# Kernel optimization log

Hardware: AMD Instinct MI355X
Metric: run time of the kernel (lower is better)

The kernel has to match this reference:

```python
import jax, jax.numpy as jnp
import numpy as np
from jax import lax

BEAM = 4
MAXLEN = 12
V, E, H = 32000, 256, 512
S, B = 512, 8


def lstm_cell(x, h, c, Wih, Whh, bih, bhh):
    # torch gate order: input, forget, cell, output
    g = x @ Wih.T + h @ Whh.T + bih + bhh
    i, f, gg, o = jnp.split(g, 4, axis=-1)
    c2 = jax.nn.sigmoid(f) * c + jax.nn.sigmoid(i) * jnp.tanh(gg)
    return jax.nn.sigmoid(o) * jnp.tanh(c2), c2


def lstm_layer(xs, Wih, Whh, bih, bhh):
    Bn, Hn = xs.shape[1], Whh.shape[1]
    h0 = jnp.zeros((Bn, Hn), xs.dtype)

    def step(carry, x):
        h, c = carry
        h, c = lstm_cell(x, h, c, Wih, Whh, bih, bhh)
        return (h, c), h

    (hT, cT), hs = lax.scan(step, (h0, h0), xs)
    return hs, hT, cT


def setup_inputs():
    key = jax.random.key(0)
    ks = jax.random.split(key, 32)

    def p(i, shape, s=0.08):
        return jax.random.normal(ks[i], shape, jnp.float32) * s

    return {
        'text': jax.random.randint(ks[0], (S, B), 0, V),
        'emb_enc': p(1, (V, E)),
        'emb_dec': p(2, (V, E)),
        'enc_Wih0': p(3, (4 * H, E)), 'enc_Whh0': p(4, (4 * H, H)),
        'enc_bih0': p(5, (4 * H,)), 'enc_bhh0': p(6, (4 * H,)),
        'enc_Wih1': p(7, (4 * H, H)), 'enc_Whh1': p(8, (4 * H, H)),
        'enc_bih1': p(9, (4 * H,)), 'enc_bhh1': p(10, (4 * H,)),
        'dec_Wih': p(11, (4 * H, E)), 'dec_Whh': p(12, (4 * H, H)),
        'dec_bih': p(13, (4 * H,)), 'dec_bhh': p(14, (4 * H,)),
        'Wq': p(15, (H, H)), 'bq': p(16, (H,)),
        'Wk': p(17, (H, H)), 'bk': p(18, (H,)),
        'Wv': p(19, (H, H)), 'bv': p(20, (H,)),
        'Wo': p(21, (H, H)), 'bo': p(22, (H,)),
        'Wout': p(23, (V, H)), 'bout': p(24, (V,)),
    }


def reference(text, emb_enc, emb_dec, enc_Wih0, enc_Whh0, enc_bih0, enc_bhh0,
              enc_Wih1, enc_Whh1, enc_bih1, enc_bhh1,
              dec_Wih, dec_Whh, dec_bih, dec_bhh,
              Wq, bq, Wk, bk, Wv, bv, Wo, bo, Wout, bout):
    # ---- encoder: 2-layer LSTM over source ----
    emb = emb_enc[text]                                   # [S, B, E]
    hs0, h0, c0 = lstm_layer(emb, enc_Wih0, enc_Whh0, enc_bih0, enc_bhh0)
    hs1, h1, c1 = lstm_layer(hs0, enc_Wih1, enc_Whh1, enc_bih1, enc_bhh1)
    enc_hidden = jnp.stack([h0, h1])                      # [L, B, H] final hidden per layer
    k_enc = enc_hidden @ Wk.T + bk                        # precompute encoder K/V projections
    v_enc = enc_hidden @ Wv.T + bv
    scale = 1.0 / jnp.sqrt(jnp.float32(H))

    # ---- beam state: all beams start from last encoder layer state ----
    dec_h = jnp.tile(h1[None], (BEAM, 1, 1))              # [BEAM, B, H]
    dec_c = jnp.tile(c1[None], (BEAM, 1, 1))
    T = MAXLEN + 1
    result = jnp.full((BEAM, T, B), 1, dtype=jnp.int32)   # SOS token = 1
    logits_hist = jnp.zeros((BEAM, T, B, V), jnp.float32).at[:, 0, :, 1].set(1.0)

    def step(carry, t):
        dh, dc, res, lh = carry
        tok = lax.dynamic_slice(res, (0, t, 0), (BEAM, 1, B))[:, 0, :]      # last token [BEAM, B]
        x = emb_dec[tok]                                                    # [BEAM, B, E]
        nh, nc = lstm_cell(x, dh, dc, dec_Wih, dec_Whh, dec_bih, dec_bhh)   # batched over beams
        # single-head attention: query = dec hidden, keys/values = [enc layers ; dec hidden]
        q = nh @ Wq.T + bq
        kd = nh @ Wk.T + bk
        vd = nh @ Wv.T + bv
        keys = jnp.concatenate([jnp.broadcast_to(k_enc[None], (BEAM,) + k_enc.shape), kd[:, None]], axis=1)  # [BEAM, L+1, B, H]
        vals = jnp.concatenate([jnp.broadcast_to(v_enc[None], (BEAM,) + v_enc.shape), vd[:, None]], axis=1)
        scores = jnp.einsum('nbh,nlbh->nbl', q, keys) * scale
        w = jax.nn.softmax(scores, axis=-1)
        ctx = jnp.einsum('nbl,nlbh->nbh', w, vals)
        dec_out = (ctx @ Wo.T + bo) @ Wout.T + bout                          # [BEAM, B, V]
        # per-beam top-k over vocab, then top-k over the BEAM*BEAM candidates
        pv, pt = lax.top_k(dec_out, BEAM)                                    # [BEAM, B, K]
        cand_v = jnp.transpose(pv, (1, 0, 2)).reshape(B, BEAM * BEAM)        # beam-major blocks
        cand_t = jnp.transpose(pt, (1, 0, 2)).reshape(B, BEAM * BEAM)
        _, ti = lax.top_k(cand_v, BEAM)                                      # [B, K]
        old_beam = (ti // BEAM).T                                            # [BEAM, B]
        new_tok = jnp.take_along_axis(cand_t, ti, axis=1).T                  # [BEAM, B]
        # vectorized beam reorder (gather) of state + history
        nh = jnp.take_along_axis(nh, old_beam[:, :, None], axis=0)
        nc = jnp.take_along_axis(nc, old_beam[:, :, None], axis=0)
        res = jnp.take_along_axis(res, old_beam[:, None, :], axis=0)
        lh = jnp.take_along_axis(lh, old_beam[:, None, :, None], axis=0)
        step_log = jnp.take_along_axis(dec_out, old_beam[:, :, None], axis=0)
        res = lax.dynamic_update_slice(res, new_tok[:, None, :].astype(jnp.int32), (0, t + 1, 0))
        lh = lax.dynamic_update_slice(lh, step_log[:, None], (0, t + 1, 0, 0))
        return (nh, nc, res, lh), None

    (dec_h, dec_c, result, logits_hist), _ = lax.scan(
        step, (dec_h, dec_c, result, logits_hist), jnp.arange(MAXLEN))
    output_res = result[0].T                               # [B, T]
    output_logits = jnp.transpose(logits_hist[0], (1, 2, 0))  # [B, V, T]
    return output_res, output_logits
```

## Files before the change

### kernel.cpp

```cpp
#include <hip/hip_runtime.h>
#include <hip/hip_bf16.h>
#include <float.h>


using ull = unsigned long long;

#define SCOPE_AGENT __HIP_MEMORY_SCOPE_AGENT

__device__ __forceinline__ float cLoad(const float* p) {
  return __hip_atomic_load(p, __ATOMIC_RELAXED, SCOPE_AGENT);
}
__device__ __forceinline__ void cStore(float* p, float v) {
  __hip_atomic_store(p, v, __ATOMIC_RELAXED, SCOPE_AGENT);
}
__device__ __forceinline__ int cLoadI(const int* p) {
  return __hip_atomic_load(p, __ATOMIC_RELAXED, SCOPE_AGENT);
}
__device__ __forceinline__ void cStoreI(int* p, int v) {
  __hip_atomic_store(p, v, __ATOMIC_RELAXED, SCOPE_AGENT);
}
__device__ __forceinline__ ull cLoad64(const ull* p) {
  return __hip_atomic_load(p, __ATOMIC_RELAXED, SCOPE_AGENT);
}
__device__ __forceinline__ void cStore64(ull* p, ull v) {
  __hip_atomic_store(p, v, __ATOMIC_RELAXED, SCOPE_AGENT);
}

__device__ __forceinline__ float2 u2f2(ull u) {
  union { ull u; float2 f; } c; c.u = u; return c.f;
}

__device__ __forceinline__ ull pollLoad(const ull* p) {
  ull v = cLoad64(p);
  while ((unsigned)v == 0xFFFFFFFFu || (unsigned)(v >> 32) == 0xFFFFFFFFu)
    v = cLoad64(p);
  return v;
}

__device__ __forceinline__ void fbar1(int* fl, int phase) {
  __syncthreads();
  if (threadIdx.x < 32)
    cStoreI(fl + (blockIdx.x * 32 + threadIdx.x) * 32, phase);
  {
    const int* f = fl + (threadIdx.x * 32 + (blockIdx.x >> 3)) * 32;
    while (cLoadI(f) < phase) {}
  }
  __syncthreads();
}

__device__ __forceinline__ float sig_(float x) { return 1.0f / (1.0f + expf(-x)); }

__device__ __forceinline__ void ins4(float* v, int* id, float nv, int ni) {
  if (nv > v[3] || (nv == v[3] && ni < id[3])) {
    v[3] = nv; id[3] = ni;
#pragma unroll
    for (int p = 3; p > 0; --p) {
      bool sw = (v[p] > v[p - 1]) || (v[p] == v[p - 1] && id[p] < id[p - 1]);
      if (sw) {
        float t0 = v[p]; v[p] = v[p - 1]; v[p - 1] = t0;
        int t1 = id[p]; id[p] = id[p - 1]; id[p - 1] = t1;
      }
    }
  }
}

struct EncP {
  const int* text; const float* emb;
  const float* Wih0; const float* Whh0; const float* bih0; const float* bhh0;
  const float* Wih1; const float* Whh1; const float* bih1; const float* bhh1;
  float* h0hist; float* h1hist;
  float* h0f; float* h1f; float* c1f;
};

template <int KX>
__device__ void enc_run(const EncP& P, float* xcat, int w, int tid) {
  constexpr int KTOT = KX + 512;
  constexpr int ST = KTOT + 4;
  constexpr int KSL = KTOT / 8;
  constexpr int Q = KSL / 4;
  constexpr int L = (KX == 512) ? 1 : 0;
  __shared__ float part[16 * 8 * 8];
  __shared__ float gl[128];

  const int c0 = (w & 127) * 4;
  const int kh = tid >> 5, col = (tid >> 3) & 3, b = tid & 7;
  const int kbase = kh * KSL;

  const float* Wih = L ? P.Wih1 : P.Wih0;
  const float* Whh = L ? P.Whh1 : P.Whh0;
  const float4* wih4[4]; const float4* whh4[4];
#pragma unroll
  for (int g = 0; g < 4; ++g) {
    const int row = g * 512 + c0 + col;
    wih4[g] = (const float4*)(Wih + (size_t)row * KX);
    whh4[g] = (const float4*)(Whh + (size_t)row * 512);
  }
  float bsum = 0.f;
  if (tid < 128) {
    const int r = tid >> 3;
    const int row = (r & 3) * 512 + c0 + (r >> 2);
    bsum = (L ? P.bih1[row] + P.bhh1[row] : P.bih0[row] + P.bhh0[row]);
  }
  float creg = 0.f;
  float* myHist = L ? P.h1hist : P.h0hist;

  int qx = (KX - kbase) / 4;
  qx = qx < 0 ? 0 : (qx > Q ? Q : qx);

  for (int e = tid; e < 4096; e += 256)
    xcat[(e >> 9) * ST + KX + (e & 511)] = 0.f;
  __syncthreads();

  for (int t = 0; t < 512; ++t) {
    if constexpr (KX == 256) {
      for (int e = tid; e < 1024; e += 256) {
        const int b2 = e >> 7, k2 = e & 127;
        const int tokv = P.text[t * 8 + b2];
        *(float2*)(xcat + b2 * ST + 2 * k2) =
            *(const float2*)(P.emb + (size_t)tokv * 256 + 2 * k2);
      }
    } else {
      const ull* x0 = (const ull*)(P.h0hist + (size_t)(t + 1) * 4096);
      for (int e = tid; e < 2048; e += 256) {
        const int b2 = e >> 8, k2 = e & 255;
        *(ull*)(xcat + b2 * ST + 2 * k2) = pollLoad(x0 + b2 * 256 + k2);
      }
    }
    if (t >= 1) {
      const ull* hq = (const ull*)(myHist + (size_t)t * 4096);
      for (int e = tid; e < 2048; e += 256) {
        const int b2 = e >> 8, k2 = e & 255;
        *(ull*)(xcat + b2 * ST + KX + 2 * k2) = pollLoad(hq + b2 * 256 + k2);
      }
    }
    __syncthreads();

    float a0 = 0.f, a1 = 0.f, a2 = 0.f, a3 = 0.f;
    {
      const float4* xq = (const float4*)(xcat + b * ST + kbase);
      const int iw = kbase >> 2, ih = (kbase - KX) >> 2;
#pragma unroll 4
      for (int q = 0; q < qx; ++q) {
        float4 x = xq[q];
        float4 w0 = wih4[0][iw + q], w1 = wih4[1][iw + q];
        float4 w2 = wih4[2][iw + q], w3 = wih4[3][iw + q];
        a0 = fmaf(w0.x, x.x, a0); a0 = fmaf(w0.y, x.y, a0);
        a0 = fmaf(w0.z, x.z, a0); a0 = fmaf(w0.w, x.w, a0);
        a1 = fmaf(w1.x, x.x, a1); a1 = fmaf(w1.y, x.y, a1);
        a1 = fmaf(w1.z, x.z, a1); a1 = fmaf(w1.w, x.w, a1);
        a2 = fmaf(w2.x, x.x, a2); a2 = fmaf(w2.y, x.y, a2);
        a2 = fmaf(w2.z, x.z, a2); a2 = fmaf(w2.w, x.w, a2);
        a3 = fmaf(w3.x, x.x, a3); a3 = fmaf(w3.y, x.y, a3);
        a3 = fmaf(w3.z, x.z, a3); a3 = fmaf(w3.w, x.w, a3);
      }
#pragma unroll 4
      for (int q = qx; q < Q; ++q) {
        float4 x = xq[q];
        float4 w0 = whh4[0][ih + q], w1 = whh4[1][ih + q];
        float4 w2 = whh4[2][ih + q], w3 = whh4[3][ih + q];
        a0 = fmaf(w0.x, x.x, a0); a0 = fmaf(w0.y, x.y, a0);
        a0 = fmaf(w0.z, x.z, a0); a0 = fmaf(w0.w, x.w, a0);
        a1 = fmaf(w1.x, x.x, a1); a1 = fmaf(w1.y, x.y, a1);
        a1 = fmaf(w1.z, x.z, a1); a1 = fmaf(w1.w, x.w, a1);
        a2 = fmaf(w2.x, x.x, a2); a2 = fmaf(w2.y, x.y, a2);
        a2 = fmaf(w2.z, x.z, a2); a2 = fmaf(w2.w, x.w, a2);
        a3 = fmaf(w3.x, x.x, a3); a3 = fmaf(w3.y, x.y, a3);
        a3 = fmaf(w3.z, x.z, a3); a3 = fmaf(w3.w, x.w, a3);
      }
    }
    part[((col * 4 + 0) * 8 + b) * 8 + kh] = a0;
    part[((col * 4 + 1) * 8 + b) * 8 + kh] = a1;
    part[((col * 4 + 2) * 8 + b) * 8 + kh] = a2;
    part[((col * 4 + 3) * 8 + b) * 8 + kh] = a3;
    __syncthreads();
    if (tid < 128) {
      const int r = tid >> 3, b2 = tid & 7;
      const float4* pp = (const float4*)(part + (r * 8 + b2) * 8);
      float4 p0 = pp[0], p1 = pp[1];
      gl[r * 8 + b2] =
          bsum + (((p0.x + p0.y) + (p0.z + p0.w)) + ((p1.x + p1.y) + (p1.z + p1.w)));
    }
    __syncthreads();
    if (tid < 32) {
      const int cc = tid >> 3, b2 = tid & 7;
      float gi = gl[(cc * 4 + 0) * 8 + b2], gf_ = gl[(cc * 4 + 1) * 8 + b2];
      float gg = gl[(cc * 4 + 2) * 8 + b2], go = gl[(cc * 4 + 3) * 8 + b2];
      float c2 = sig_(gf_) * creg + sig_(gi) * tanhf(gg);
      float hv = sig_(go) * tanhf(c2);
      creg = c2;
      cStore(myHist + (size_t)(t + 1) * 4096 + b2 * 512 + c0 + cc, hv);
      if (t == 511) {
        (L ? P.h1f : P.h0f)[b2 * 512 + c0 + cc] = hv;
        if (L) P.c1f[b2 * 512 + c0 + cc] = c2;
      }
    }
    __syncthreads();
  }
}

__global__ __launch_bounds__(256, 1) void enc_kernel(EncP P) {
  __shared__ float xcat0[8 * 772];
  __shared__ float xcat1[8 * 1028];
  if (blockIdx.x >> 7) enc_run<512>(P, xcat1, blockIdx.x, threadIdx.x);
  else enc_run<256>(P, xcat0, blockIdx.x, threadIdx.x);
}

__global__ __launch_bounds__(256) void prep_kernel(
    const float* Wk, const float* bk, const float* Wv, const float* bv,
    const float* h0f, const float* h1f, const float* c1f,
    float* kenc, float* venc, float* nhb, float* ncb) {
  const int w = blockIdx.x, tid = threadIdx.x;
  if (w < 64) {
    const int o = w * 256 + tid;
    const int kv = o >> 13, l = (o >> 12) & 1, b = (o >> 9) & 7, c = o & 511;
    const float4* h4 = (const float4*)((l ? h1f : h0f) + b * 512);
    const float4* w4 = (const float4*)((kv ? Wv : Wk) + (size_t)c * 512);
    float s0 = 0.f, s1 = 0.f, s2 = 0.f, s3 = 0.f;
#pragma unroll 8
    for (int k = 0; k < 128; ++k) {
      float4 a = w4[k], x = h4[k];
      s0 = fmaf(a.x, x.x, s0); s1 = fmaf(a.y, x.y, s1);
      s2 = fmaf(a.z, x.z, s2); s3 = fmaf(a.w, x.w, s3);
    }
    (kv ? venc : kenc)[l * 4096 + b * 512 + c] =
        (kv ? bv : bk)[c] + ((s0 + s1) + (s2 + s3));
  } else {
    const int o = (w - 64) * 256 + tid;
    nhb[16384 + o] = h1f[o & 4095];
    ncb[16384 + o] = c1f[o & 4095];
  }
}

__global__ __launch_bounds__(256) void prep2_kernel(
    const float* Wq, const float* Wk, const float* Wv, const float* Wo,
    const float* bq, const float* bk, const float* bv,
    const float* kenc, const float* venc,
    float* At, float* W2, float* u, float* pvec, float* veWo, float* bvo,
    float* sl0, float* sbb) {
  const int w = blockIdx.x, tid = threadIdx.x;
#pragma unroll 1
  for (int sub = 0; sub < 2; ++sub) {
    const int d = 2 * w + sub;
    for (int cc = 0; cc < 2; ++cc) {
      const int c = tid + cc * 256;
      float s0 = 0.f, s1 = 0.f, s2 = 0.f, s3 = 0.f;
      for (int i = 0; i < 512; i += 4) {
        s0 = fmaf(Wk[(i + 0) * 512 + d], Wq[(i + 0) * 512 + c], s0);
        s1 = fmaf(Wk[(i + 1) * 512 + d], Wq[(i + 1) * 512 + c], s1);
        s2 = fmaf(Wk[(i + 2) * 512 + d], Wq[(i + 2) * 512 + c], s2);
        s3 = fmaf(Wk[(i + 3) * 512 + d], Wq[(i + 3) * 512 + c], s3);
      }
      At[(size_t)d * 512 + c] = (s0 + s1) + (s2 + s3);
    }
    for (int cc = 0; cc < 2; ++cc) {
      const int dc = tid + cc * 256;
      float s0 = 0.f, s1 = 0.f, s2 = 0.f, s3 = 0.f;
      const float* wor = Wo + (size_t)d * 512;
      for (int c2 = 0; c2 < 512; c2 += 4) {
        s0 = fmaf(wor[c2 + 0], Wv[(size_t)(c2 + 0) * 512 + dc], s0);
        s1 = fmaf(wor[c2 + 1], Wv[(size_t)(c2 + 1) * 512 + dc], s1);
        s2 = fmaf(wor[c2 + 2], Wv[(size_t)(c2 + 2) * 512 + dc], s2);
        s3 = fmaf(wor[c2 + 3], Wv[(size_t)(c2 + 3) * 512 + dc], s3);
      }
      W2[(size_t)d * 512 + dc] = (s0 + s1) + (s2 + s3);
    }
  }
  if (w == 0) {
    for (int cc = 0; cc < 2; ++cc) {
      const int c = tid + cc * 256;
      float a = 0.f;
      for (int i = 0; i < 512; ++i)
        a += Wq[i * 512 + c] * bk[i] + Wk[i * 512 + c] * bq[i];
      u[c] = a;
    }
  } else if (w <= 32) {
    const int idx = (w - 1) * 256 + tid;
    const int l = idx >> 12, b = (idx >> 9) & 7, c = idx & 511;
    const float* ke = kenc + l * 4096 + b * 512;
    float a = 0.f;
    for (int i = 0; i < 512; ++i) a = fmaf(Wq[i * 512 + c], ke[i], a);
    pvec[idx] = a;
  } else if (w <= 64) {
    const int idx = (w - 33) * 256 + tid;
    const int l = idx >> 12, b = (idx >> 9) & 7, j = idx & 511;
    const float* ve = venc + l * 4096 + b * 512;
    const float* wo = Wo + (size_t)j * 512;
    float a = 0.f;
    for (int c = 0; c < 512; ++c) a = fmaf(wo[c], ve[c], a);
    veWo[idx] = a;
  } else if (w == 65) {
    for (int cc = 0; cc < 2; ++cc) {
      const int j = tid + cc * 256;
      const float* wo = Wo + (size_t)j * 512;
      float a = 0.f;
      for (int c = 0; c < 512; ++c) a = fmaf(wo[c], bv[c], a);
      bvo[j] = a;
    }
  } else if (w == 66) {
    if (tid < 16) {
      const int l = tid >> 3, b = tid & 7;
      const float* ke = kenc + l * 4096 + b * 512;
      float a = 0.f;
      for (int i = 0; i < 512; ++i) a = fmaf(bq[i], ke[i], a);
      sl0[tid] = a;
    } else if (tid == 16) {
      float a = 0.f;
      for (int i = 0; i < 512; ++i) a = fmaf(bq[i], bk[i], a);
      sbb[0] = a;
    }
  }
}

__global__ __launch_bounds__(256) void prep3_kernel(
    const float* Wout, const float* bout, const float* bo, const float* veWo,
    float* E0g, float* E1g, float* bcg) {
  __shared__ float sv[16 * 516 + 512];
  __shared__ float stg[8 * 516];
  const int w = blockIdx.x, tid = threadIdx.x;
  for (int e = tid; e < 8704; e += 256) {
    if (e < 8192) sv[(e >> 9) * 516 + (e & 511)] = veWo[e];
    else sv[16 * 516 + (e - 8192)] = bo[e - 8192];
  }
  const int cbase = w * 125;
  for (int tile = 0; tile < 16; ++tile) {
    const int r0 = tile * 8;
    __syncthreads();
    for (int e = tid; e < 1024; e += 256) {
      const int rr = e >> 7, k4 = e & 127;
      int row = r0 + rr; if (row > 124) row = 124;
      *(float4*)&stg[rr * 516 + k4 * 4] =
          *(const float4*)&Wout[(size_t)(cbase + row) * 512 + k4 * 4];
    }
    __syncthreads();
    if (tid < 136) {
      const int rr = tid / 17, sel = tid - rr * 17;
      const int row = r0 + rr;
      if (row < 125) {
        const float4* a4 = (const float4*)&stg[rr * 516];
        const float4* x4 =
            (const float4*)&sv[sel < 16 ? sel * 516 : 16 * 516];
        float s0 = 0.f, s1 = 0.f, s2 = 0.f, s3 = 0.f;
#pragma unroll 8
        for (int k = 0; k < 128; ++k) {
          float4 a = a4[k], x = x4[k];
          s0 = fmaf(a.x, x.x, s0); s1 = fmaf(a.y, x.y, s1);
          s2 = fmaf(a.z, x.z, s2); s3 = fmaf(a.w, x.w, s3);
        }
        const float s = (s0 + s1) + (s2 + s3);
        const int c = cbase + row;
        if (sel < 16) (sel < 8 ? E0g : E1g)[(size_t)(sel & 7) * 32000 + c] = s;
        else bcg[c] = s + bout[c];
      }
    }
  }
}

struct DecP {
  const float* emb;
  const float* Wih; const float* Whh; const float* bih; const float* bhh;
  const float* Wout;
  const float* At; const float* W2; const float* u; const float* bvo;
  const float* pvec; const float* sl0; const float* sbb;
  const float* E0g; const float* E1g; const float* bcg;
  float* nhb; float* ncb;
  float* vbuf;
  float* part_s;
  ull* pvp;
  int* obh;
  int* res0;
  __hip_bfloat16* hist;
  int* fl;
};

__global__ __launch_bounds__(256, 1) void dec_kernel(DecP P) {
  __shared__ float SM[29600];
  __shared__ float gl[2][4][32];
  __shared__ float slS[32][3];
  __shared__ float wslS[96];
  __shared__ float svv[32][8][4];
  __shared__ int sii[32][8][4];
  __shared__ float rvS[32][4];
  __shared__ int rtS[32][4];
  __shared__ int resS[4][13][8];
  __shared__ int oblS[32];
  __shared__ int tokS[32];
  __shared__ float pscS[32][8];
  __shared__ float nhsS[32][8];

  const int w = blockIdx.x, tid = threadIdx.x;
  float* hs = SM;
  float* tileS = SM;
  float* vqS = SM + 16896;
  float* tvE = SM + 21120;
  int* tiE = (int*)(SM + 25344);
  int ph = 0;

  if (tid < 104) {
    for (int n = 0; n < 4; ++n) resS[n][tid >> 3][tid & 7] = 1;
  }

  auto do_select = [&](int tt) {
    {
      const int r = tid >> 3, ch = tid & 7;
      float m4[4] = {-FLT_MAX, -FLT_MAX, -FLT_MAX, -FLT_MAX};
      int mi[4] = {0x7fffffff, 0x7fffffff, 0x7fffffff, 0x7fffffff};
      for (int g = 0; g < 4; ++g) {
        ull pk[32];
#pragma unroll
        for (int z = 0; z < 32; ++z) {
          const int wg = ch * 32 + g * 8 + (z >> 2);
          pk[z] = cLoad64(P.pvp + wg * 128 + r * 4 + (z & 3));
        }
#pragma unroll
        for (int z = 0; z < 32; ++z)
          ins4(m4, mi, __uint_as_float((unsigned)(pk[z] >> 32)),
               (int)(unsigned)(pk[z] & 0xffffffffu));
      }
#pragma unroll
      for (int k = 0; k < 4; ++k) { svv[r][ch][k] = m4[k]; sii[r][ch][k] = mi[k]; }
    }
    __syncthreads();
    if (tid < 32) {
      float m4[4] = {-FLT_MAX, -FLT_MAX, -FLT_MAX, -FLT_MAX};
      int mi[4] = {0x7fffffff, 0x7fffffff, 0x7fffffff, 0x7fffffff};
      for (int g2 = 0; g2 < 8; ++g2)
#pragma unroll
        for (int k = 0; k < 4; ++k) ins4(m4, mi, svv[tid][g2][k], sii[tid][g2][k]);
#pragma unroll
      for (int k = 0; k < 4; ++k) { rvS[tid][k] = m4[k]; rtS[tid][k] = mi[k]; }
    }
    __syncthreads();
    if (tid < 8) {
      const int b2 = tid;
      unsigned used = 0;
      int obl_[4], tkl_[4];
#pragma unroll
      for (int sel = 0; sel < 4; ++sel) {
        float bestv = -FLT_MAX; int bestj = -1;
        for (int j = 0; j < 16; ++j) {
          if (used & (1u << j)) continue;
          float vv = rvS[(j >> 2) * 8 + b2][j & 3];
          if (vv > bestv) { bestv = vv; bestj = j; }
        }
        used |= 1u << bestj;
        const int obn = bestj >> 2;
        obl_[sel] = obn;
        tkl_[sel] = rtS[obn * 8 + b2][bestj & 3];
        oblS[sel * 8 + b2] = obn;
        tokS[sel * 8 + b2] = tkl_[sel];
        if (w == 0) P.obh[tt * 32 + sel * 8 + b2] = obn;
      }
      if (w == 0) {
        int tmp[4][13];
        for (int n2 = 0; n2 < 4; ++n2)
          for (int s2 = 0; s2 < 13; ++s2) tmp[n2][s2] = resS[obl_[n2]][s2][b2];
        for (int n2 = 0; n2 < 4; ++n2)
          for (int s2 = 0; s2 < 13; ++s2) resS[n2][s2][b2] = tmp[n2][s2];
        for (int n2 = 0; n2 < 4; ++n2) resS[n2][tt + 1][b2] = tkl_[n2];
      }
    }
    __syncthreads();
    if (tt == 11 && w == 0 && tid < 104)
      P.res0[tid] = resS[0][tid >> 3][tid & 7];
  };

  for (int t = 0; t < 12; ++t) {
    const int curOff = (t & 1) * 16384, prevOff = ((t + 1) & 1) * 16384;

    if (t == 0) {
      __syncthreads();
      if (tid < 32) { oblS[tid] = tid >> 3; tokS[tid] = 1; }
      __syncthreads();
    } else {
      do_select(t - 1);
    }
    {
      const int col_l = tid >> 7, gate = (tid >> 5) & 3, nb = tid & 31;
      const int col = 2 * w + col_l;
      const int row = gate * 512 + col;
      for (int e = tid; e < 2048; e += 256) {
        const int nb2 = e >> 6, kf = e & 63;
        float4 v = *((const float4*)(P.emb + (size_t)tokS[nb2] * 256) + kf);
        *((float4*)hs + nb2 * 65 + kf) = v;
      }
      __syncthreads();
      float s0 = 0.f, s1 = 0.f, s2 = 0.f, s3 = 0.f;
      {
        const float4* a4 = (const float4*)(P.Wih + (size_t)row * 256);
        const float4* x4 = (const float4*)hs + nb * 65;
#pragma unroll 8
        for (int k = 0; k < 64; ++k) {
          float4 a = a4[k], x = x4[k];
          s0 = fmaf(a.x, x.x, s0); s1 = fmaf(a.y, x.y, s1);
          s2 = fmaf(a.z, x.z, s2); s3 = fmaf(a.w, x.w, s3);
        }
      }
      float acc = P.bih[row] + P.bhh[row];
      const ull* hsrc = (const ull*)(P.nhb + prevOff);
      const float4* w4row = (const float4*)(P.Whh + (size_t)row * 512);
      for (int ck = 0; ck < 2; ++ck) {
        __syncthreads();
        for (int e = tid; e < 4096; e += 256) {
          const int nb2 = e >> 7, k2 = e & 127;
          const int srow = oblS[nb2] * 8 + (nb2 & 7);
          ull v = cLoad64(hsrc + srow * 256 + ck * 128 + k2);
          *(ull*)(hs + nb2 * 260 + 2 * k2) = v;
        }
        __syncthreads();
        const float4* h4 = (const float4*)hs + nb * 65;
        const float4* w4 = w4row + ck * 64;
#pragma unroll 8
        for (int k = 0; k < 64; ++k) {
          float4 a = w4[k], x = h4[k];
          s0 = fmaf(a.x, x.x, s0); s1 = fmaf(a.y, x.y, s1);
          s2 = fmaf(a.z, x.z, s2); s3 = fmaf(a.w, x.w, s3);
        }
      }
      acc += (s0 + s1) + (s2 + s3);
      gl[col_l][gate][nb] = acc;
      __syncthreads();
      if (tid < 64) {
        const int cc = tid >> 5, nb2 = tid & 31;
        const int col2 = 2 * w + cc;
        float gi = gl[cc][0][nb2], gf_ = gl[cc][1][nb2];
        float gg = gl[cc][2][nb2], go = gl[cc][3][nb2];
        const int srow = oblS[nb2] * 8 + (nb2 & 7);
        float cold = cLoad(P.ncb + prevOff + srow * 512 + col2);
        float c2 = sig_(gf_) * cold + sig_(gi) * tanhf(gg);
        float hv = sig_(go) * tanhf(c2);
        cStore(P.nhb + curOff + nb2 * 512 + col2, hv);
        cStore(P.ncb + curOff + nb2 * 512 + col2, c2);
      }
    }
    fbar1(P.fl, ++ph);

    if (w < 128) {
      const int p = w >> 6, cb = w & 63;
      const int col_l = tid >> 5, nb = tid & 31;
      const int col = cb * 8 + col_l;
      const float* W = (p ? P.W2 : P.At) + (size_t)col * 512;
      float acc = (p ? P.bvo : P.u)[col];
      {
        const float4* w4row = (const float4*)W;
        float s0 = 0.f, s1 = 0.f, s2 = 0.f, s3 = 0.f;
        for (int ck = 0; ck < 2; ++ck) {
          __syncthreads();
          const ull* s8 = (const ull*)(P.nhb + curOff);
          for (int e = tid; e < 4096; e += 256) {
            const int nb2 = e >> 7, k2 = e & 127;
            ull v = cLoad64(s8 + nb2 * 256 + ck * 128 + k2);
            *(ull*)(hs + nb2 * 260 + 2 * k2) = v;
          }
          __syncthreads();
          const float4* h4 = (const float4*)hs + nb * 65;
          const float4* w4 = w4row + ck * 64;
#pragma unroll 8
          for (int k = 0; k < 64; ++k) {
            float4 a = w4[k], x = h4[k];
            s0 = fmaf(a.x, x.x, s0); s1 = fmaf(a.y, x.y, s1);
            s2 = fmaf(a.z, x.z, s2); s3 = fmaf(a.w, x.w, s3);
          }
        }
        acc += (s0 + s1) + (s2 + s3);
      }
      if (p) {
        cStore(P.vbuf + nb * 512 + col, acc);
      } else {
        const float nhv = cLoad(P.nhb + curOff + nb * 512 + col);
        pscS[nb][col_l] = nhv * acc;
        nhsS[nb][col_l] = nhv;
        __syncthreads();
        if (tid < 32) {
          const int nb2 = tid, b = nb2 & 7;
          float s2a = 0.f, l0 = 0.f, l1 = 0.f;
#pragma unroll
          for (int i2 = 0; i2 < 8; ++i2) {
            s2a += pscS[nb2][i2];
            const float nv = nhsS[nb2][i2];
            l0 = fmaf(nv, P.pvec[b * 512 + cb * 8 + i2], l0);
            l1 = fmaf(nv, P.pvec[4096 + b * 512 + cb * 8 + i2], l1);
          }
          cStore(P.part_s + (0 * 32 + nb2) * 64 + cb, l0);
          cStore(P.part_s + (1 * 32 + nb2) * 64 + cb, l1);
          cStore(P.part_s + (2 * 32 + nb2) * 64 + cb, s2a);
        }
      }
    }
    fbar1(P.fl, ++ph);

    {
      const int cbase = w * 125;
      if (tid < 96) {
        const int nb = tid / 3, l = tid - (tid / 3) * 3, b = nb & 7;
        const ull* ps = (const ull*)(P.part_s + (l * 32 + nb) * 64);
        ull pk[32];
#pragma unroll
        for (int z = 0; z < 32; ++z) pk[z] = cLoad64(ps + z);
        float s = 0.f;
#pragma unroll
        for (int z = 0; z < 32; ++z) { float2 f = u2f2(pk[z]); s += f.x + f.y; }
        const float bias = (l < 2) ? P.sl0[l * 8 + b] : P.sbb[0];
        slS[nb][l] = (s + bias) * (1.0f / sqrtf(512.0f));
      }
      __syncthreads();
      if (tid < 32) {
        float a = slS[tid][0], b2 = slS[tid][1], c3 = slS[tid][2];
        float m = fmaxf(a, fmaxf(b2, c3));
        float e0 = expf(a - m), e1 = expf(b2 - m), e2 = expf(c3 - m);
        float inv = 1.0f / (e0 + e1 + e2);
        wslS[tid * 3 + 0] = e0 * inv;
        wslS[tid * 3 + 1] = e1 * inv;
        wslS[tid * 3 + 2] = e2 * inv;
      }
      const int rg = tid >> 3, ng = tid & 7;
      float acc[4][4];
#pragma unroll
      for (int i = 0; i < 4; ++i)
#pragma unroll
        for (int j = 0; j < 4; ++j) acc[i][j] = 0.f;
      for (int q = 0; q < 4; ++q) {
        __syncthreads();
        for (int e = tid; e < 1024; e += 256) {
          const int nb = e >> 5, kf = e & 31;
          ull u0 = cLoad64((const ull*)(P.vbuf + nb * 512 + q * 128 + kf * 4));
          ull u1 = cLoad64((const ull*)(P.vbuf + nb * 512 + q * 128 + kf * 4 + 2));
          float2 a = u2f2(u0), b2 = u2f2(u1);
          float4 v = {a.x, a.y, b2.x, b2.y};
          *(float4*)(vqS + (nb & 3) * 1056 + (nb >> 2) * 132 + kf * 4) = v;
        }
        for (int it = 0; it < 16; ++it) {
          const int idx = it * 256 + tid;
          if (idx < 4000) {
            const int r = idx >> 5, kf = idx & 31;
            float4 v = *(const float4*)(P.Wout + (size_t)(cbase + r) * 512 +
                                        q * 128 + kf * 4);
            *(float4*)(tileS + (r & 3) * 4224 + (r >> 2) * 132 + kf * 4) = v;
          }
        }
        __syncthreads();
        for (int kf = 0; kf < 32; ++kf) {
          float4 xv[4], wv[4];
#pragma unroll
          for (int j = 0; j < 4; ++j)
            xv[j] = *(const float4*)(vqS + j * 1056 + ng * 132 + kf * 4);
#pragma unroll
          for (int i = 0; i < 4; ++i)
            wv[i] = *(const float4*)(tileS + i * 4224 + rg * 132 + kf * 4);
#pragma unroll
          for (int i = 0; i < 4; ++i)
#pragma unroll
            for (int j = 0; j < 4; ++j) {
              float a = acc[i][j];
              a = fmaf(wv[i].x, xv[j].x, a); a = fmaf(wv[i].y, xv[j].y, a);
              a = fmaf(wv[i].z, xv[j].z, a); a = fmaf(wv[i].w, xv[j].w, a);
              acc[i][j] = a;
            }
        }
      }
      __syncthreads();
      float w0w[4], w1w[4], w2w[4];
#pragma unroll
      for (int j = 0; j < 4; ++j) {
        const int nb = ng * 4 + j;
        w0w[j] = wslS[nb * 3 + 0]; w1w[j] = wslS[nb * 3 + 1]; w2w[j] = wslS[nb * 3 + 2];
      }
      float v4[4][4]; int i4[4][4];
#pragma unroll
      for (int j = 0; j < 4; ++j)
#pragma unroll
        for (int k = 0; k < 4; ++k) { v4[j][k] = -FLT_MAX; i4[j][k] = 0x7fffffff; }
#pragma unroll
      for (int i = 0; i < 4; ++i) {
        const int r = rg * 4 + i;
        if (r < 125) {
          const int c = cbase + r;
          const float bcv = P.bcg[c];
#pragma unroll
          for (int j = 0; j < 4; ++j) {
            const int nb = ng * 4 + j, b = nb & 7;
            const float e0 = P.E0g[(size_t)b * 32000 + c];
            const float e1 = P.E1g[(size_t)b * 32000 + c];
            const float L = fmaf(w2w[j], acc[i][j],
                                 fmaf(w0w[j], e0, fmaf(w1w[j], e1, bcv)));
            P.hist[(size_t)t * 1024000 + (size_t)nb * 32000 + c] = __float2bfloat16(L);
            ins4(v4[j], i4[j], L, c);
          }
        }
      }
#pragma unroll
      for (int j = 0; j < 4; ++j)
#pragma unroll
        for (int k = 0; k < 4; ++k) {
          tvE[(ng * 4 + j) * 132 + rg * 4 + k] = v4[j][k];
          tiE[(ng * 4 + j) * 132 + rg * 4 + k] = i4[j][k];
        }
      __syncthreads();
      if (tid < 32) {
        float m4[4] = {-FLT_MAX, -FLT_MAX, -FLT_MAX, -FLT_MAX};
        int mi[4] = {0x7fffffff, 0x7fffffff, 0x7fffffff, 0x7fffffff};
        for (int e = 0; e < 128; ++e)
          ins4(m4, mi, tvE[tid * 132 + e], tiE[tid * 132 + e]);
#pragma unroll
        for (int k = 0; k < 4; ++k) {
          ull pk = ((ull)__float_as_uint(m4[k]) << 32) | (unsigned)mi[k];
          cStore64(P.pvp + w * 128 + tid * 4 + k, pk);
        }
      }
    }
    fbar1(P.fl, ++ph);
  }
  if (w == 0) do_select(11);
}

__global__ __launch_bounds__(256) void out_kernel(const __hip_bfloat16* hist,
                                                  const int* obh, const int* res0,
                                                  float* out) {
  __shared__ float sh[13 * 1000];
  __shared__ int sbArr[12];
  const int w = blockIdx.x, tid = threadIdx.x;
  const int b = w >> 5, v0 = (w & 31) * 1000;
  if (tid == 0) {
    int beta = 0;
    for (int t = 11; t >= 0; --t) {
      const int sb = obh[t * 32 + beta * 8 + b];
      sbArr[t] = sb;
      beta = sb;
    }
  }
  __syncthreads();
  for (int e = tid; e < 12000; e += 256) {
    const int t = e / 1000, vv = e - t * 1000;
    sh[(t + 1) * 1000 + vv] = __bfloat162float(
        hist[(size_t)(t * 32 + sbArr[t] * 8 + b) * 32000 + v0 + vv]);
  }
  for (int e = tid; e < 1000; e += 256) sh[e] = (v0 + e == 1) ? 1.0f : 0.0f;
  __syncthreads();
  float* base = out + 104 + (size_t)(b * 32000 + v0) * 13;
  for (int o = tid; o < 13000; o += 256) {
    const int v = o / 13, t = o - v * 13;
    base[o] = sh[t * 1000 + v];
  }
  if (w == 0 && tid < 104) {
    out[(tid & 7) * 13 + (tid >> 3)] = (float)res0[tid];
  }
}

extern "C" void kernel_launch(void* const* d_in, const int* in_sizes, int n_in,
                              void* d_out, int out_size, void* d_ws, size_t ws_size,
                              hipStream_t stream) {
  const int* text  = (const int*)d_in[0];
  const float* embE = (const float*)d_in[1];
  const float* embD = (const float*)d_in[2];
  const float* Wih0 = (const float*)d_in[3];
  const float* Whh0 = (const float*)d_in[4];
  const float* bih0 = (const float*)d_in[5];
  const float* bhh0 = (const float*)d_in[6];
  const float* Wih1 = (const float*)d_in[7];
  const float* Whh1 = (const float*)d_in[8];
  const float* bih1 = (const float*)d_in[9];
  const float* bhh1 = (const float*)d_in[10];
  const float* dWih = (const float*)d_in[11];
  const float* dWhh = (const float*)d_in[12];
  const float* dbih = (const float*)d_in[13];
  const float* dbhh = (const float*)d_in[14];
  const float* Wq = (const float*)d_in[15];
  const float* bq = (const float*)d_in[16];
  const float* Wk = (const float*)d_in[17];
  const float* bk = (const float*)d_in[18];
  const float* Wv = (const float*)d_in[19];
  const float* bv = (const float*)d_in[20];
  const float* Wo = (const float*)d_in[21];
  const float* bo = (const float*)d_in[22];
  const float* Wout = (const float*)d_in[23];
  const float* bout = (const float*)d_in[24];

  char* ws = (char*)d_ws;
  size_t off = 0;
  auto alloc = [&](size_t bytes) -> char* {
    off = (off + 511) & ~(size_t)511;
    char* p = ws + off;
    off += bytes;
    return p;
  };
  float* h0hist = (float*)alloc((size_t)513 * 4096 * 4);
  float* h1hist = (float*)alloc((size_t)513 * 4096 * 4);
  int* decFl  = (int*)alloc((size_t)262144 * 4);
  float* h0f  = (float*)alloc(4096 * 4);
  float* h1f  = (float*)alloc(4096 * 4);
  float* c1f  = (float*)alloc(4096 * 4);
  float* kenc = (float*)alloc(8192 * 4);
  float* venc = (float*)alloc(8192 * 4);
  float* At   = (float*)alloc((size_t)262144 * 4);
  float* W2   = (float*)alloc((size_t)262144 * 4);
  float* u    = (float*)alloc(512 * 4);
  float* pvec = (float*)alloc(8192 * 4);
  float* veWo = (float*)alloc(8192 * 4);
  float* bvo  = (float*)alloc(512 * 4);
  float* sl0  = (float*)alloc(16 * 4);
  float* sbb  = (float*)alloc(32 * 4);
  float* E0g  = (float*)alloc((size_t)256000 * 4);
  float* E1g  = (float*)alloc((size_t)256000 * 4);
  float* bcg  = (float*)alloc(32000 * 4);
  float* nhb  = (float*)alloc(2 * 16384 * 4);
  float* ncb  = (float*)alloc(2 * 16384 * 4);
  float* vbuf = (float*)alloc(16384 * 4);
  float* part_s = (float*)alloc(6144 * 4);
  ull* pvp    = (ull*)alloc((size_t)32768 * 8);
  int* obh    = (int*)alloc(384 * 4);
  int* res0   = (int*)alloc(104 * 4);
  __hip_bfloat16* hist = (__hip_bfloat16*)alloc((size_t)12288000 * 2);
  if (off > ws_size) return;

  hipMemsetAsync(h0hist, 0xFF, (size_t)513 * 4096 * 4, stream);
  hipMemsetAsync(h1hist, 0xFF, (size_t)513 * 4096 * 4, stream);
  hipMemsetAsync(decFl, 0, (size_t)262144 * 4, stream);

  EncP ep{text, embE, Wih0, Whh0, bih0, bhh0, Wih1, Whh1, bih1, bhh1,
          h0hist, h1hist, h0f, h1f, c1f};
  enc_kernel<<<256, 256, 0, stream>>>(ep);

  prep_kernel<<<128, 256, 0, stream>>>(Wk, bk, Wv, bv, h0f, h1f, c1f, kenc, venc,
                                       nhb, ncb);
  prep2_kernel<<<256, 256, 0, stream>>>(Wq, Wk, Wv, Wo, bq, bk, bv, kenc, venc,
                                        At, W2, u, pvec, veWo, bvo, sl0, sbb);
  prep3_kernel<<<256, 256, 0, stream>>>(Wout, bout, bo, veWo, E0g, E1g, bcg);

  DecP dp{embD, dWih, dWhh, dbih, dbhh, Wout,
          At, W2, u, bvo, pvec, sl0, sbb, E0g, E1g, bcg,
          nhb, ncb, vbuf, part_s, pvp, obh, res0, hist, decFl};
  dec_kernel<<<256, 256, 0, stream>>>(dp);

  out_kernel<<<256, 256, 0, stream>>>(hist, obh, res0, (float*)d_out);
}
```

Measured before the change: 6.623 ms.

## Replace sentinel polling with flag barrier and replicated double-buffered hidden state

The encoder's per-element sentinel polling on a 513-step history buffer is replaced with a flag-based global barrier. Hidden states now go into small double-buffered arrays, replicated 16x for layer 0 and 8x for layer 1, so groups of blocks read separate copies and contention drops. Layer 1 runs one step behind layer 0 in lockstep. The k-split reduction moves from shared-memory partials plus two syncthreads to intra-wavefront shuffles. In exchange, each block does more global stores per step and every step waits on a full barrier.

```diff
diff --git a/kernel.cpp b/kernel.cpp
--- a/kernel.cpp
+++ b/kernel.cpp
@@ -28,13 +28,6 @@
 
 __device__ __forceinline__ float2 u2f2(ull u) {
   union { ull u; float2 f; } c; c.u = u; return c.f;
-}
-
-__device__ __forceinline__ ull pollLoad(const ull* p) {
-  ull v = cLoad64(p);
-  while ((unsigned)v == 0xFFFFFFFFu || (unsigned)(v >> 32) == 0xFFFFFFFFu)
-    v = cLoad64(p);
-  return v;
 }
 
 __device__ __forceinline__ void fbar1(int* fl, int phase) {
@@ -68,7 +61,7 @@
   const int* text; const float* emb;
   const float* Wih0; const float* Whh0; const float* bih0; const float* bhh0;
   const float* Wih1; const float* Whh1; const float* bih1; const float* bhh1;
-  float* h0hist; float* h1hist;
+  float* h0rep; float* h1rep; int* regF;
   float* h0f; float* h1f; float* c1f;
 };
 
@@ -76,125 +69,139 @@
 __device__ void enc_run(const EncP& P, float* xcat, int w, int tid) {
   constexpr int KTOT = KX + 512;
   constexpr int ST = KTOT + 4;
-  constexpr int KSL = KTOT / 8;
-  constexpr int Q = KSL / 4;
+  constexpr int Q = KTOT / 32;
+  constexpr int QX = KX / 32;
   constexpr int L = (KX == 512) ? 1 : 0;
-  __shared__ float part[16 * 8 * 8];
-  __shared__ float gl[128];
+  constexpr int NR = L ? 8 : 16;
 
   const int c0 = (w & 127) * 4;
-  const int kh = tid >> 5, col = (tid >> 3) & 3, b = tid & 7;
-  const int kbase = kh * KSL;
+  const int kh = tid & 7, col = (tid >> 3) & 3, b = tid >> 5;
+  const int frep = w >> 3;
+  const int drep = (w & 127) >> 4;
 
   const float* Wih = L ? P.Wih1 : P.Wih0;
   const float* Whh = L ? P.Whh1 : P.Whh0;
   const float4* wih4[4]; const float4* whh4[4];
+  float bias4[4];
 #pragma unroll
   for (int g = 0; g < 4; ++g) {
     const int row = g * 512 + c0 + col;
     wih4[g] = (const float4*)(Wih + (size_t)row * KX);
     whh4[g] = (const float4*)(Whh + (size_t)row * 512);
-  }
-  float bsum = 0.f;
-  if (tid < 128) {
-    const int r = tid >> 3;
-    const int row = (r & 3) * 512 + c0 + (r >> 2);
-    bsum = (L ? P.bih1[row] + P.bhh1[row] : P.bih0[row] + P.bhh0[row]);
+    bias4[g] = L ? (P.bih1[row] + P.bhh1[row]) : (P.bih0[row] + P.bhh0[row]);
   }
   float creg = 0.f;
-  float* myHist = L ? P.h1hist : P.h0hist;
-
-  int qx = (KX - kbase) / 4;
-  qx = qx < 0 ? 0 : (qx > Q ? Q : qx);
+  float* myRep = L ? P.h1rep : P.h0rep;
 
   for (int e = tid; e < 4096; e += 256)
     xcat[(e >> 9) * ST + KX + (e & 511)] = 0.f;
   __syncthreads();
 
-  for (int t = 0; t < 512; ++t) {
-    if constexpr (KX == 256) {
-      for (int e = tid; e < 1024; e += 256) {
-        const int b2 = e >> 7, k2 = e & 127;
-        const int tokv = P.text[t * 8 + b2];
-        *(float2*)(xcat + b2 * ST + 2 * k2) =
-            *(const float2*)(P.emb + (size_t)tokv * 256 + 2 * k2);
-      }
-    } else {
-      const ull* x0 = (const ull*)(P.h0hist + (size_t)(t + 1) * 4096);
-      for (int e = tid; e < 2048; e += 256) {
-        const int b2 = e >> 8, k2 = e & 255;
-        *(ull*)(xcat + b2 * ST + 2 * k2) = pollLoad(x0 + b2 * 256 + k2);
-      }
-    }
-    if (t >= 1) {
-      const ull* hq = (const ull*)(myHist + (size_t)t * 4096);
-      for (int e = tid; e < 2048; e += 256) {
-        const int b2 = e >> 8, k2 = e & 255;
-        *(ull*)(xcat + b2 * ST + KX + 2 * k2) = pollLoad(hq + b2 * 256 + k2);
-      }
-    }
-    __syncthreads();
-
-    float a0 = 0.f, a1 = 0.f, a2 = 0.f, a3 = 0.f;
-    {
-      const float4* xq = (const float4*)(xcat + b * ST + kbase);
-      const int iw = kbase >> 2, ih = (kbase - KX) >> 2;
+  for (int i = 0; i <= 512; ++i) {
+    const bool act = L ? (i >= 1) : (i < 512);
+    if (act) {
+      const int t = L ? (i - 1) : i;
+      if constexpr (KX == 256) {
+        for (int e = tid; e < 1024; e += 256) {
+          const int b2 = e >> 7, k2 = e & 127;
+          const int tokv = P.text[t * 8 + b2];
+          *(float2*)(xcat + b2 * ST + 2 * k2) =
+              *(const float2*)(P.emb + (size_t)tokv * 256 + 2 * k2);
+        }
+      }
+      if (i >= 1) {
+        const int s = tid;
+        if ((s < 128) || (i >= 2)) {
+          const int* f = P.regF + (s * 32 + frep) * 32;
+          while (cLoadI(f) < i) {}
+        }
+      }
+      __syncthreads();
+      if constexpr (KX == 256) {
+        if (i >= 1) {
+          const ull* src = (const ull*)(P.h0rep +
+              (size_t)(((i + 1) & 1) * 16 + drep) * 4096);
+          for (int e = tid; e < 2048; e += 256) {
+            const int b2 = e >> 8, k2 = e & 255;
+            *(ull*)(xcat + b2 * ST + KX + 2 * k2) = cLoad64(src + b2 * 256 + k2);
+          }
+        }
+      } else {
+        {
+          const ull* src = (const ull*)(P.h0rep +
+              (size_t)(((i + 1) & 1) * 16 + 8 + drep) * 4096);
+          for (int e = tid; e < 2048; e += 256) {
+            const int b2 = e >> 8, k2 = e & 255;
+            *(ull*)(xcat + b2 * ST + 2 * k2) = cLoad64(src + b2 * 256 + k2);
+          }
+        }
+        if (i >= 2) {
+          const ull* src = (const ull*)(P.h1rep +
+              (size_t)((i & 1) * 8 + drep) * 4096);
+          for (int e = tid; e < 2048; e += 256) {
+            const int b2 = e >> 8, k2 = e & 255;
+            *(ull*)(xcat + b2 * ST + KX + 2 * k2) = cLoad64(src + b2 * 256 + k2);
+          }
+        }
+      }
+      __syncthreads();
+      float a0 = 0.f, a1 = 0.f, a2 = 0.f, a3 = 0.f;
+      {
+        const float4* xq = (const float4*)(xcat + b * ST);
 #pragma unroll 4
-      for (int q = 0; q < qx; ++q) {
-        float4 x = xq[q];
-        float4 w0 = wih4[0][iw + q], w1 = wih4[1][iw + q];
-        float4 w2 = wih4[2][iw + q], w3 = wih4[3][iw + q];
-        a0 = fmaf(w0.x, x.x, a0); a0 = fmaf(w0.y, x.y, a0);
-        a0 = fmaf(w0.z, x.z, a0); a0 = fmaf(w0.w, x.w, a0);
-        a1 = fmaf(w1.x, x.x, a1); a1 = fmaf(w1.y, x.y, a1);
-        a1 = fmaf(w1.z, x.z, a1); a1 = fmaf(w1.w, x.w, a1);
-        a2 = fmaf(w2.x, x.x, a2); a2 = fmaf(w2.y, x.y, a2);
-        a2 = fmaf(w2.z, x.z, a2); a2 = fmaf(w2.w, x.w, a2);
-        a3 = fmaf(w3.x, x.x, a3); a3 = fmaf(w3.y, x.y, a3);
-        a3 = fmaf(w3.z, x.z, a3); a3 = fmaf(w3.w, x.w, a3);
-      }
+        for (int q = 0; q < QX; ++q) {
+          const int c4 = q * 8 + kh;
+          float4 x = xq[c4];
+          float4 w0 = wih4[0][c4], w1 = wih4[1][c4];
+          float4 w2 = wih4[2][c4], w3 = wih4[3][c4];
+          a0 = fmaf(w0.x, x.x, a0); a0 = fmaf(w0.y, x.y, a0);
+          a0 = fmaf(w0.z, x.z, a0); a0 = fmaf(w0.w, x.w, a0);
+          a1 = fmaf(w1.x, x.x, a1); a1 = fmaf(w1.y, x.y, a1);
+          a1 = fmaf(w1.z, x.z, a1); a1 = fmaf(w1.w, x.w, a1);
+          a2 = fmaf(w2.x, x.x, a2); a2 = fmaf(w2.y, x.y, a2);
+          a2 = fmaf(w2.z, x.z, a2); a2 = fmaf(w2.w, x.w, a2);
+          a3 = fmaf(w3.x, x.x, a3); a3 = fmaf(w3.y, x.y, a3);
+          a3 = fmaf(w3.z, x.z, a3); a3 = fmaf(w3.w, x.w, a3);
+        }
 #pragma unroll 4
-      for (int q = qx; q < Q; ++q) {
-        float4 x = xq[q];
-        float4 w0 = whh4[0][ih + q], w1 = whh4[1][ih + q];
-        float4 w2 = whh4[2][ih + q], w3 = whh4[3][ih + q];
-        a0 = fmaf(w0.x, x.x, a0); a0 = fmaf(w0.y, x.y, a0);
-        a0 = fmaf(w0.z, x.z, a0); a0 = fmaf(w0.w, x.w, a0);
-        a1 = fmaf(w1.x, x.x, a1); a1 = fmaf(w1.y, x.y, a1);
-        a1 = fmaf(w1.z, x.z, a1); a1 = fmaf(w1.w, x.w, a1);
-        a2 = fmaf(w2.x, x.x, a2); a2 = fmaf(w2.y, x.y, a2);
-        a2 = fmaf(w2.z, x.z, a2); a2 = fmaf(w2.w, x.w, a2);
-        a3 = fmaf(w3.x, x.x, a3); a3 = fmaf(w3.y, x.y, a3);
-        a3 = fmaf(w3.z, x.z, a3); a3 = fmaf(w3.w, x.w, a3);
-      }
-    }
-    part[((col * 4 + 0) * 8 + b) * 8 + kh] = a0;
-    part[((col * 4 + 1) * 8 + b) * 8 + kh] = a1;
-    part[((col * 4 + 2) * 8 + b) * 8 + kh] = a2;
-    part[((col * 4 + 3) * 8 + b) * 8 + kh] = a3;
-    __syncthreads();
-    if (tid < 128) {
-      const int r = tid >> 3, b2 = tid & 7;
-      const float4* pp = (const float4*)(part + (r * 8 + b2) * 8);
-      float4 p0 = pp[0], p1 = pp[1];
-      gl[r * 8 + b2] =
-          bsum + (((p0.x + p0.y) + (p0.z + p0.w)) + ((p1.x + p1.y) + (p1.z + p1.w)));
-    }
-    __syncthreads();
-    if (tid < 32) {
-      const int cc = tid >> 3, b2 = tid & 7;
-      float gi = gl[(cc * 4 + 0) * 8 + b2], gf_ = gl[(cc * 4 + 1) * 8 + b2];
-      float gg = gl[(cc * 4 + 2) * 8 + b2], go = gl[(cc * 4 + 3) * 8 + b2];
-      float c2 = sig_(gf_) * creg + sig_(gi) * tanhf(gg);
-      float hv = sig_(go) * tanhf(c2);
-      creg = c2;
-      cStore(myHist + (size_t)(t + 1) * 4096 + b2 * 512 + c0 + cc, hv);
-      if (t == 511) {
-        (L ? P.h1f : P.h0f)[b2 * 512 + c0 + cc] = hv;
-        if (L) P.c1f[b2 * 512 + c0 + cc] = c2;
-      }
-    }
-    __syncthreads();
+        for (int q = QX; q < Q; ++q) {
+          const int c4 = q * 8 + kh;
+          const int h4i = c4 - (KX >> 2);
+          float4 x = xq[c4];
+          float4 w0 = whh4[0][h4i], w1 = whh4[1][h4i];
+          float4 w2 = whh4[2][h4i], w3 = whh4[3][h4i];
+          a0 = fmaf(w0.x, x.x, a0); a0 = fmaf(w0.y, x.y, a0);
+          a0 = fmaf(w0.z, x.z, a0); a0 = fmaf(w0.w, x.w, a0);
+          a1 = fmaf(w1.x, x.x, a1); a1 = fmaf(w1.y, x.y, a1);
+          a1 = fmaf(w1.z, x.z, a1); a1 = fmaf(w1.w, x.w, a1);
+          a2 = fmaf(w2.x, x.x, a2); a2 = fmaf(w2.y, x.y, a2);
+          a2 = fmaf(w2.z, x.z, a2); a2 = fmaf(w2.w, x.w, a2);
+          a3 = fmaf(w3.x, x.x, a3); a3 = fmaf(w3.y, x.y, a3);
+          a3 = fmaf(w3.z, x.z, a3); a3 = fmaf(w3.w, x.w, a3);
+        }
+      }
+      a0 += __shfl_xor(a0, 1); a0 += __shfl_xor(a0, 2); a0 += __shfl_xor(a0, 4);
+      a1 += __shfl_xor(a1, 1); a1 += __shfl_xor(a1, 2); a1 += __shfl_xor(a1, 4);
+      a2 += __shfl_xor(a2, 1); a2 += __shfl_xor(a2, 2); a2 += __shfl_xor(a2, 4);
+      a3 += __shfl_xor(a3, 1); a3 += __shfl_xor(a3, 2); a3 += __shfl_xor(a3, 4);
+      if (kh == 0) {
+        const float gi = a0 + bias4[0], gf_ = a1 + bias4[1];
+        const float gg = a2 + bias4[2], go = a3 + bias4[3];
+        const float c2 = sig_(gf_) * creg + sig_(gi) * tanhf(gg);
+        const float hv = sig_(go) * tanhf(c2);
+        creg = c2;
+        const int p = t & 1;
+        float* dst = myRep + (size_t)p * NR * 4096 + b * 512 + c0 + col;
+#pragma unroll
+        for (int r = 0; r < NR; ++r) cStore(dst + (size_t)r * 4096, hv);
+        if (t == 511) {
+          (L ? P.h1f : P.h0f)[b * 512 + c0 + col] = hv;
+          if (L) P.c1f[b * 512 + c0 + col] = c2;
+        }
+      }
+      __syncthreads();
+      if (tid < 32) cStoreI(P.regF + (w * 32 + tid) * 32, i + 1);
+    }
   }
 }
 
@@ -782,8 +789,9 @@
     off += bytes;
     return p;
   };
-  float* h0hist = (float*)alloc((size_t)513 * 4096 * 4);
-  float* h1hist = (float*)alloc((size_t)513 * 4096 * 4);
+  float* h0rep = (float*)alloc((size_t)2 * 16 * 4096 * 4);
+  float* h1rep = (float*)alloc((size_t)2 * 8 * 4096 * 4);
+  int* regF   = (int*)alloc((size_t)262144 * 4);
   int* decFl  = (int*)alloc((size_t)262144 * 4);
   float* h0f  = (float*)alloc(4096 * 4);
   float* h1f  = (float*)alloc(4096 * 4);
@@ -811,12 +819,11 @@
   __hip_bfloat16* hist = (__hip_bfloat16*)alloc((size_t)12288000 * 2);
   if (off > ws_size) return;
 
-  hipMemsetAsync(h0hist, 0xFF, (size_t)513 * 4096 * 4, stream);
-  hipMemsetAsync(h1hist, 0xFF, (size_t)513 * 4096 * 4, stream);
+  hipMemsetAsync(regF, 0, (size_t)262144 * 4, stream);
   hipMemsetAsync(decFl, 0, (size_t)262144 * 4, stream);
 
   EncP ep{text, embE, Wih0, Whh0, bih0, bhh0, Wih1, Whh1, bih1, bhh1,
-          h0hist, h1hist, h0f, h1f, c1f};
+          h0rep, h1rep, regF, h0f, h1f, c1f};
   enc_kernel<<<256, 256, 0, stream>>>(ep);
 
   prep_kernel<<<128, 256, 0, stream>>>(Wk, bk, Wv, bv, h0f, h1f, c1f, kenc, venc,
```

After: 7.674 ms. 15.9% more time.
